# Kernel tuning notes

Hardware: AMD Instinct MI355X
Metric: run time of the kernel (lower is better)

## Reference

```python
import jax, jax.numpy as jnp
import numpy as np

G = 128          # voxel grid extent per axis
KS = 3           # kernel size per axis
KK = KS ** 3     # 27 kernel offsets
N_IN, N_OUT, C_IN, C_OUT = 50000, 100000, 128, 128


def setup_inputs() -> dict:
    key = jax.random.key(0)
    k1, k2, k3, k4 = jax.random.split(key, 4)
    features = jax.random.normal(k1, (N_IN, C_IN), dtype=jnp.float32)
    W = jax.random.normal(k2, (KK, C_IN, C_OUT), dtype=jnp.float32) * (1.0 / np.sqrt(C_IN * KK))
    inp_positions = jax.random.randint(k3, (N_IN, 3), 0, G, dtype=jnp.int32)
    out_positions = jax.random.randint(k4, (N_OUT, 3), 0, G, dtype=jnp.int32)
    return {"features": features, "W": W,
            "inp_positions": inp_positions, "out_positions": out_positions}


def _kernel_offsets():
    r = np.arange(KS) - KS // 2  # [-1, 0, 1] for KS=3 (offset=0 since KS is odd)
    dx, dy, dz = np.meshgrid(r, r, r, indexing="ij")
    return jnp.asarray(np.stack([dx.ravel(), dy.ravel(), dz.ravel()], axis=1), dtype=jnp.int32)  # [KK,3]


def reference(features, W, inp_positions, out_positions):
    # Sparse conv-transpose: voxelize input points (voxel_size=1, offset=0 -> identity
    # on integer coords), build voxel->input-index hash (dense grid table), then for
    # each output point gather the input feature at each of the KK kernel offsets and
    # accumulate W[k'] @ feat with mirrored kernel index (transpose of SparseConv).
    lin_in = (inp_positions[:, 0] * G + inp_positions[:, 1]) * G + inp_positions[:, 2]
    grid = jnp.full((G * G * G,), -1, dtype=jnp.int32)
    grid = grid.at[lin_in].max(jnp.arange(N_IN, dtype=jnp.int32))  # deterministic on dup voxels

    offsets = _kernel_offsets()          # [KK, 3]
    W_mirror = W[::-1]                   # transpose conv uses mirrored kernel index

    def step(acc, xk):
        off, Wk = xk                     # off [3], Wk [C_IN, C_OUT]
        nb = out_positions + off[None, :]               # [N_OUT, 3]
        in_bounds = jnp.all((nb >= 0) & (nb < G), axis=1)
        lin = (nb[:, 0] * G + nb[:, 1]) * G + nb[:, 2]
        idx = grid[jnp.clip(lin, 0, G * G * G - 1)]      # [N_OUT]
        ok = in_bounds & (idx >= 0)
        f = jnp.where(ok[:, None], features[jnp.clip(idx, 0)], 0.0)  # [N_OUT, C_IN]
        return acc + f @ Wk, None

    acc0 = jnp.zeros((out_positions.shape[0], W.shape[2]), dtype=features.dtype)
    out, _ = jax.lax.scan(step, acc0, (offsets, W_mirror))
    return out
```

## Files before the change

### kernel.cpp

```cpp
#include <hip/hip_runtime.h>
#include <hip/hip_bf16.h>

#define G    128
#define GGG  (G * G * G)
#define C    128
#define KK   27
#define CAP  4096
#define RT   16

typedef __attribute__((ext_vector_type(8))) short bf16x8;
typedef __attribute__((ext_vector_type(4))) float f32x4;

__device__ __forceinline__ ushort f2b(float f) {
    __hip_bfloat16 h = __float2bfloat16(f);
    return *reinterpret_cast<ushort*>(&h);
}

__global__ void prep_kernel(int4* __restrict__ grid4, int* __restrict__ cnt,
                            const float* __restrict__ W, ushort* __restrict__ Wtb) {
    int tid = blockIdx.x * blockDim.x + threadIdx.x;
    int stride = gridDim.x * blockDim.x;
    int4 mone = {-1, -1, -1, -1};
    for (int i = tid; i < GGG / 4; i += stride) grid4[i] = mone;
    if (tid < KK) cnt[tid] = 0;
    const int NW = KK * C * C;
    for (int i = tid; i < NW; i += stride) {
        int m = i >> 14;
        int r = i & 16383;
        int co = r >> 7, ci = r & 127;
        Wtb[i] = f2b(W[(size_t)(KK - 1 - m) * C * C + ci * C + co]);
    }
}

__global__ void scatter_kernel(const int* __restrict__ pos,
                               int* __restrict__ grid, int n) {
    int i = blockIdx.x * blockDim.x + threadIdx.x;
    if (i >= n) return;
    int x = pos[3 * i], y = pos[3 * i + 1], z = pos[3 * i + 2];
    atomicMax(&grid[(x * G + y) * G + z], i);
}

__global__ __launch_bounds__(256) void compact3b_kernel(
    const int* __restrict__ out_pos, const int* __restrict__ grid,
    int* __restrict__ cnt, int* __restrict__ pairs,
    int* __restrict__ cnt_row, int* __restrict__ rowtap, int n_out)
{
    int row = blockIdx.x * 256 + threadIdx.x;
    bool valid = row < n_out;
    int lane = threadIdx.x & 63;

    int px = 0, py = 0, pz = 0;
    if (valid) { px = out_pos[3*row]; py = out_pos[3*row+1]; pz = out_pos[3*row+2]; }

    int idx[KK];
#pragma unroll
    for (int m = 0; m < KK; ++m) {
        int x = px + m / 9 - 1, y = py + (m % 9) / 3 - 1, z = pz + m % 3 - 1;
        bool inb = valid && (unsigned)x < G && (unsigned)y < G && (unsigned)z < G;
        idx[m] = inb ? grid[(x * G + y) * G + z] : -1;
    }

    __shared__ int bcnt[KK], bbase[KK];
    if (threadIdx.x < KK) bcnt[threadIdx.x] = 0;
    __syncthreads();

    int gl[KK];
#pragma unroll
    for (int m = 0; m < KK; ++m) {
        unsigned long long act = __ballot(idx[m] >= 0);
        int lpre = __popcll(act & ((1ull << lane) - 1ull));
        int wcnt = __popcll(act);
        int wbase = 0;
        if (lane == 0 && wcnt) wbase = atomicAdd(&bcnt[m], wcnt);
        wbase = __shfl(wbase, 0);
        gl[m] = wbase + lpre;
    }
    __syncthreads();
    if (threadIdx.x < KK) bbase[threadIdx.x] = atomicAdd(&cnt[threadIdx.x], bcnt[threadIdx.x]);
    __syncthreads();

    int cr = 0;
#pragma unroll
    for (int m = 0; m < KK; ++m) {
        int g = -1;
        if (idx[m] >= 0) {
            g = bbase[m] + gl[m];
            if (g < CAP) pairs[m * CAP + g] = idx[m];
            else g = -1;
        }
        if (g >= 0 && cr < RT) {
            rowtap[cr * n_out + row] = (g << 5) | m;
            ++cr;
        }
    }
    if (valid) cnt_row[row] = cr;
}

__global__ __launch_bounds__(256, 3) void pair_mm3_kernel(
    const float* __restrict__ features, const ushort* __restrict__ Wtb,
    const int* __restrict__ pairs, const int* __restrict__ cnt,
    ushort* __restrict__ part)
{
    int m = blockIdx.y;
    int nm = min(cnt[m], CAP);
    if ((int)(blockIdx.x * 64) >= nm) return;

    __shared__ ushort Wl[128 * 136];
    __shared__ ushort Af[64 * 136];
    __shared__ int    idx_s[64];

    {
        const uint4* src = (const uint4*)(Wtb + (size_t)m * C * C);
        uint4* dst = (uint4*)Wl;
        for (int q = threadIdx.x; q < 2048; q += 256) {
            int r = q >> 4, c = q & 15;
            dst[r * 17 + c] = src[q];
        }
    }

    int lane = threadIdx.x & 63;
    int w    = threadIdx.x >> 6;
    int l15  = lane & 15;
    int quad = lane >> 4;
    const float4* fg4 = (const float4*)features;

    for (int base = blockIdx.x * 64; base < nm; base += gridDim.x * 64) {
        __syncthreads();
        if (threadIdx.x < 64) {
            int g = base + threadIdx.x;
            idx_s[threadIdx.x] = (g < nm) ? pairs[m * CAP + g] : -1;
        }
        __syncthreads();

#pragma unroll
        for (int k = 0; k < 8; ++k) {
            int q = threadIdx.x + k * 256;
            int r = q >> 5, c4 = q & 31;
            int id = idx_s[r];
            if (id >= 0) {
                float4 v = fg4[(size_t)id * 32 + c4];
                union { ushort u[4]; uint2 p; } pk;
                pk.u[0] = f2b(v.x); pk.u[1] = f2b(v.y);
                pk.u[2] = f2b(v.z); pk.u[3] = f2b(v.w);
                *(uint2*)&Af[r * 136 + c4 * 4] = pk.p;
            }
        }
        __syncthreads();

        f32x4 acc[8];
#pragma unroll
        for (int n = 0; n < 8; ++n) acc[n] = (f32x4){0.f, 0.f, 0.f, 0.f};

        int arow = 16 * w + l15;
#pragma unroll
        for (int kk = 0; kk < 4; ++kk) {
            bf16x8 a = *(bf16x8*)&Af[arow * 136 + kk * 32 + quad * 8];
#pragma unroll
            for (int n = 0; n < 8; ++n) {
                bf16x8 b = *(bf16x8*)&Wl[(n * 16 + l15) * 136 + kk * 32 + quad * 8];
                acc[n] = __builtin_amdgcn_mfma_f32_16x16x32_bf16(a, b, acc[n], 0, 0, 0);
            }
        }

        int r0 = 16 * w + quad * 4;
#pragma unroll
        for (int n = 0; n < 8; ++n) {
#pragma unroll
            for (int reg = 0; reg < 4; ++reg) {
                int r = r0 + reg;
                if (base + r < nm)
                    part[((size_t)(m * CAP + base + r)) * C + n * 16 + l15] =
                        f2b(acc[n][reg]);
            }
        }
    }
}

__global__ __launch_bounds__(256) void gather_sum2_kernel(
    const ushort* __restrict__ part, const int* __restrict__ rowtap,
    const int* __restrict__ cnt_row, float* __restrict__ out, int n_out)
{
    int row0 = blockIdx.x * 16;
    int rl = threadIdx.x >> 4;
    int t  = threadIdx.x & 15;
    int row = row0 + rl;

    __shared__ int rt_s[RT][16];
    __shared__ int cnt_s[16];
    if (threadIdx.x < 16) {
        int r = row0 + threadIdx.x;
        cnt_s[threadIdx.x] = (r < n_out) ? cnt_row[r] : 0;
    }
    {
        int q = threadIdx.x;
        int k = q >> 4, r = q & 15;
        rt_s[k][r] = (row0 + r < n_out) ? rowtap[k * n_out + row0 + r] : 0;
    }
    __syncthreads();

    int nt = cnt_s[rl];
    float acc[8] = {0,0,0,0,0,0,0,0};
    for (int k = 0; k < nt; ++k) {
        int e = rt_s[k][rl];
        int m = e & 31, g = e >> 5;
        uint4 v = *(const uint4*)(part + ((size_t)(m * CAP + g)) * C + t * 8);
        acc[0] += __uint_as_float(v.x << 16);
        acc[1] += __uint_as_float(v.x & 0xffff0000u);
        acc[2] += __uint_as_float(v.y << 16);
        acc[3] += __uint_as_float(v.y & 0xffff0000u);
        acc[4] += __uint_as_float(v.z << 16);
        acc[5] += __uint_as_float(v.z & 0xffff0000u);
        acc[6] += __uint_as_float(v.w << 16);
        acc[7] += __uint_as_float(v.w & 0xffff0000u);
    }
    if (row < n_out) {
        float* o = out + (size_t)row * C + t * 8;
        *(float4*)(o)     = (float4){acc[0], acc[1], acc[2], acc[3]};
        *(float4*)(o + 4) = (float4){acc[4], acc[5], acc[6], acc[7]};
    }
}

__global__ void init2_kernel(int4* __restrict__ grid4, int* __restrict__ cnt) {
    int i = blockIdx.x * blockDim.x + threadIdx.x;
    int stride = gridDim.x * blockDim.x;
    int4 mone = {-1, -1, -1, -1};
    for (int j = i; j < GGG / 4; j += stride) grid4[j] = mone;
    if (i < KK) cnt[i] = 0;
}

__global__ __launch_bounds__(128) void gather_mm_kernel(
    const float* __restrict__ features, const float* __restrict__ W,
    const int* __restrict__ out_pos, const int* __restrict__ grid,
    float* __restrict__ out, int n_out)
{
    int row = blockIdx.x;
    if (row >= n_out) return;
    int c = threadIdx.x;
    __shared__ int   nb_idx[KK];
    __shared__ float feat_s[C];
    int px = out_pos[3*row], py = out_pos[3*row+1], pz = out_pos[3*row+2];
    if (c < KK) {
        int i = c / 9, j = (c % 9) / 3, k = c % 3;
        int x = px + i - 1, y = py + j - 1, z = pz + k - 1;
        int idx = -1;
        if ((unsigned)x < G && (unsigned)y < G && (unsigned)z < G)
            idx = grid[(x * G + y) * G + z];
        nb_idx[c] = idx;
    }
    __syncthreads();
    float acc = 0.f;
    for (int m = 0; m < KK; ++m) {
        int idx = nb_idx[m];
        if (idx < 0) continue;
        __syncthreads();
        feat_s[c] = features[idx * C + c];
        __syncthreads();
        const float* __restrict__ Wk = W + (KK - 1 - m) * C * C + c;
        float a = 0.f;
#pragma unroll
        for (int ci = 0; ci < C; ++ci) a += feat_s[ci] * Wk[ci * C];
        acc += a;
    }
    out[row * C + c] = acc;
}

extern "C" void kernel_launch(void* const* d_in, const int* in_sizes, int n_in,
                              void* d_out, int out_size, void* d_ws, size_t ws_size,
                              hipStream_t stream) {
    const float* features = (const float*)d_in[0];
    const float* W        = (const float*)d_in[1];
    const int*   inp_pos  = (const int*)d_in[2];
    const int*   out_pos  = (const int*)d_in[3];
    float*       out      = (float*)d_out;

    int n_in_pts  = in_sizes[2] / 3;
    int n_out_pts = out_size / C;

    size_t o_grid   = 0;
    size_t o_cnt    = (size_t)GGG * 4;
    size_t o_pairs  = (o_cnt + 256 + 255) & ~(size_t)255;
    size_t o_cntr   = (o_pairs + (size_t)KK * CAP * 4 + 255) & ~(size_t)255;
    size_t o_rowtap = (o_cntr + (size_t)n_out_pts * 4 + 255) & ~(size_t)255;
    size_t o_wtb    = (o_rowtap + (size_t)RT * n_out_pts * 4 + 255) & ~(size_t)255;
    size_t o_part   = (o_wtb + (size_t)KK * C * C * 2 + 255) & ~(size_t)255;
    size_t need     = o_part + (size_t)KK * CAP * C * 2;

    int*    grid    = (int*)((char*)d_ws + o_grid);
    int*    cnt     = (int*)((char*)d_ws + o_cnt);
    int*    pairs   = (int*)((char*)d_ws + o_pairs);
    int*    cnt_row = (int*)((char*)d_ws + o_cntr);
    int*    rowtap  = (int*)((char*)d_ws + o_rowtap);
    ushort* Wtb     = (ushort*)((char*)d_ws + o_wtb);
    ushort* part    = (ushort*)((char*)d_ws + o_part);

    if (ws_size < need) {
        hipLaunchKernelGGL(init2_kernel, dim3(2048), dim3(256), 0, stream,
                           (int4*)grid, cnt);
        hipLaunchKernelGGL(scatter_kernel, dim3((n_in_pts + 255) / 256), dim3(256), 0, stream,
                           inp_pos, grid, n_in_pts);
        hipLaunchKernelGGL(gather_mm_kernel, dim3(n_out_pts), dim3(128), 0, stream,
                           features, W, out_pos, grid, out, n_out_pts);
        return;
    }

    hipLaunchKernelGGL(prep_kernel, dim3(1024), dim3(256), 0, stream,
                       (int4*)grid, cnt, W, Wtb);
    hipLaunchKernelGGL(scatter_kernel, dim3((n_in_pts + 255) / 256), dim3(256), 0, stream,
                       inp_pos, grid, n_in_pts);
    hipLaunchKernelGGL(compact3b_kernel, dim3((n_out_pts + 255) / 256), dim3(256), 0, stream,
                       out_pos, grid, cnt, pairs, cnt_row, rowtap, n_out_pts);
    hipLaunchKernelGGL(pair_mm3_kernel, dim3(40, KK), dim3(256), 0, stream,
                       features, Wtb, pairs, cnt, part);
    hipLaunchKernelGGL(gather_sum2_kernel, dim3((n_out_pts + 15) / 16), dim3(256), 0, stream,
                       part, rowtap, cnt_row, out, n_out_pts);
}
```

Before: 144.1 us.

## Shrink voxel grid to 16-bit and write single-tap rows directly to output

The voxel-to-input hash grid now stores 16-bit indices, written with a CAS-based 16-bit atomic max, which halves the grid memset and the lookup footprint. The pair list carries a destination row for output rows that have exactly one contributing tap. The MFMA kernel writes those rows straight to the fp32 output, skipping the bf16 partial buffer and the gather-sum pass for them. The gather kernel now loads only as many rowtap entries as the block's busiest row needs and skips single-tap rows. The 16-bit index assumes fewer than 65535 input points and uses CAS loops on shared words.

```diff
diff --git a/kernel.cpp b/kernel.cpp
--- a/kernel.cpp
+++ b/kernel.cpp
@@ -16,12 +16,12 @@
     return *reinterpret_cast<ushort*>(&h);
 }
 
-__global__ void prep_kernel(int4* __restrict__ grid4, int* __restrict__ cnt,
+__global__ void prep_kernel(uint4* __restrict__ grid16_4, int* __restrict__ cnt,
                             const float* __restrict__ W, ushort* __restrict__ Wtb) {
     int tid = blockIdx.x * blockDim.x + threadIdx.x;
     int stride = gridDim.x * blockDim.x;
-    int4 mone = {-1, -1, -1, -1};
-    for (int i = tid; i < GGG / 4; i += stride) grid4[i] = mone;
+    uint4 ffff = {0xFFFFFFFFu, 0xFFFFFFFFu, 0xFFFFFFFFu, 0xFFFFFFFFu};
+    for (int i = tid; i < GGG * 2 / 16; i += stride) grid16_4[i] = ffff;
     if (tid < KK) cnt[tid] = 0;
     const int NW = KK * C * C;
     for (int i = tid; i < NW; i += stride) {
@@ -32,17 +32,28 @@
     }
 }
 
-__global__ void scatter_kernel(const int* __restrict__ pos,
-                               int* __restrict__ grid, int n) {
+__global__ void scatter16_kernel(const int* __restrict__ pos,
+                                 unsigned int* __restrict__ gword, int n) {
     int i = blockIdx.x * blockDim.x + threadIdx.x;
     if (i >= n) return;
     int x = pos[3 * i], y = pos[3 * i + 1], z = pos[3 * i + 2];
-    atomicMax(&grid[(x * G + y) * G + z], i);
-}
-
-__global__ __launch_bounds__(256) void compact3b_kernel(
-    const int* __restrict__ out_pos, const int* __restrict__ grid,
-    int* __restrict__ cnt, int* __restrict__ pairs,
+    int lin = (x * G + y) * G + z;
+    unsigned int* w = &gword[lin >> 1];
+    int sh = (lin & 1) * 16;
+    unsigned int val = (unsigned int)i;
+    unsigned int old = *w, assumed;
+    do {
+        unsigned int cur = (old >> sh) & 0xFFFFu;
+        if (cur != 0xFFFFu && cur >= val) break;
+        unsigned int nw = (old & ~(0xFFFFu << sh)) | (val << sh);
+        assumed = old;
+        old = atomicCAS(w, assumed, nw);
+    } while (old != assumed);
+}
+
+__global__ __launch_bounds__(256) void compact4_kernel(
+    const int* __restrict__ out_pos, const ushort* __restrict__ grid16,
+    int* __restrict__ cnt, int2* __restrict__ pairs,
     int* __restrict__ cnt_row, int* __restrict__ rowtap, int n_out)
 {
     int row = blockIdx.x * 256 + threadIdx.x;
@@ -57,7 +68,8 @@
     for (int m = 0; m < KK; ++m) {
         int x = px + m / 9 - 1, y = py + (m % 9) / 3 - 1, z = pz + m % 3 - 1;
         bool inb = valid && (unsigned)x < G && (unsigned)y < G && (unsigned)z < G;
-        idx[m] = inb ? grid[(x * G + y) * G + z] : -1;
+        int v = inb ? (int)grid16[(x * G + y) * G + z] : 0xFFFF;
+        idx[m] = (v == 0xFFFF) ? -1 : v;
     }
 
     __shared__ int bcnt[KK], bbase[KK];
@@ -79,27 +91,36 @@
     if (threadIdx.x < KK) bbase[threadIdx.x] = atomicAdd(&cnt[threadIdx.x], bcnt[threadIdx.x]);
     __syncthreads();
 
+    int gs[KK];
     int cr = 0;
 #pragma unroll
     for (int m = 0; m < KK; ++m) {
         int g = -1;
         if (idx[m] >= 0) {
             g = bbase[m] + gl[m];
-            if (g < CAP) pairs[m * CAP + g] = idx[m];
-            else g = -1;
-        }
-        if (g >= 0 && cr < RT) {
-            rowtap[cr * n_out + row] = (g << 5) | m;
-            ++cr;
+            if (g >= CAP) g = -1;
+        }
+        gs[m] = g;
+        if (g >= 0) ++cr;
+    }
+
+    int dest = (cr == 1) ? row : -1;
+    int k = 0;
+#pragma unroll
+    for (int m = 0; m < KK; ++m) {
+        int g = gs[m];
+        if (g >= 0) {
+            pairs[m * CAP + g] = make_int2(idx[m], dest);
+            if (k < RT) { rowtap[k * n_out + row] = (g << 5) | m; ++k; }
         }
     }
     if (valid) cnt_row[row] = cr;
 }
 
-__global__ __launch_bounds__(256, 3) void pair_mm3_kernel(
+__global__ __launch_bounds__(256, 3) void pair_mm4_kernel(
     const float* __restrict__ features, const ushort* __restrict__ Wtb,
-    const int* __restrict__ pairs, const int* __restrict__ cnt,
-    ushort* __restrict__ part)
+    const int2* __restrict__ pairs, const int* __restrict__ cnt,
+    ushort* __restrict__ part, float* __restrict__ out)
 {
     int m = blockIdx.y;
     int nm = min(cnt[m], CAP);
@@ -108,6 +129,7 @@
     __shared__ ushort Wl[128 * 136];
     __shared__ ushort Af[64 * 136];
     __shared__ int    idx_s[64];
+    __shared__ int    dest_s[64];
 
     {
         const uint4* src = (const uint4*)(Wtb + (size_t)m * C * C);
@@ -128,7 +150,9 @@
         __syncthreads();
         if (threadIdx.x < 64) {
             int g = base + threadIdx.x;
-            idx_s[threadIdx.x] = (g < nm) ? pairs[m * CAP + g] : -1;
+            int2 pr = (g < nm) ? pairs[m * CAP + g] : make_int2(-1, -1);
+            idx_s[threadIdx.x]  = pr.x;
+            dest_s[threadIdx.x] = pr.y;
         }
         __syncthreads();
 
@@ -164,19 +188,24 @@
 
         int r0 = 16 * w + quad * 4;
 #pragma unroll
-        for (int n = 0; n < 8; ++n) {
-#pragma unroll
-            for (int reg = 0; reg < 4; ++reg) {
-                int r = r0 + reg;
-                if (base + r < nm)
-                    part[((size_t)(m * CAP + base + r)) * C + n * 16 + l15] =
-                        f2b(acc[n][reg]);
+        for (int reg = 0; reg < 4; ++reg) {
+            int r = r0 + reg;
+            if (base + r >= nm) continue;
+            int d = dest_s[r];
+            if (d >= 0) {
+                float* o = out + (size_t)d * C + l15;
+#pragma unroll
+                for (int n = 0; n < 8; ++n) o[n * 16] = acc[n][reg];
+            } else {
+                ushort* p = part + ((size_t)(m * CAP + base + r)) * C + l15;
+#pragma unroll
+                for (int n = 0; n < 8; ++n) p[n * 16] = f2b(acc[n][reg]);
             }
         }
     }
 }
 
-__global__ __launch_bounds__(256) void gather_sum2_kernel(
+__global__ __launch_bounds__(256) void gather_sum3_kernel(
     const ushort* __restrict__ part, const int* __restrict__ rowtap,
     const int* __restrict__ cnt_row, float* __restrict__ out, int n_out)
 {
@@ -187,18 +216,29 @@
 
     __shared__ int rt_s[RT][16];
     __shared__ int cnt_s[16];
+    __shared__ int maxc;
     if (threadIdx.x < 16) {
         int r = row0 + threadIdx.x;
         cnt_s[threadIdx.x] = (r < n_out) ? cnt_row[r] : 0;
     }
+    __syncthreads();
+    if (threadIdx.x == 0) {
+        int mx = 0;
+#pragma unroll
+        for (int i = 0; i < 16; ++i) mx = max(mx, cnt_s[i]);
+        maxc = mx;
+    }
+    __syncthreads();
     {
-        int q = threadIdx.x;
-        int k = q >> 4, r = q & 15;
-        rt_s[k][r] = (row0 + r < n_out) ? rowtap[k * n_out + row0 + r] : 0;
+        int k = threadIdx.x >> 4, r = threadIdx.x & 15;
+        if (k < maxc)
+            rt_s[k][r] = (row0 + r < n_out) ? rowtap[k * n_out + row0 + r] : 0;
     }
     __syncthreads();
 
     int nt = cnt_s[rl];
+    if (nt == 1) return;
+
     float acc[8] = {0,0,0,0,0,0,0,0};
     for (int k = 0; k < nt; ++k) {
         int e = rt_s[k][rl];
@@ -226,6 +266,14 @@
     int4 mone = {-1, -1, -1, -1};
     for (int j = i; j < GGG / 4; j += stride) grid4[j] = mone;
     if (i < KK) cnt[i] = 0;
+}
+
+__global__ void scatter_kernel(const int* __restrict__ pos,
+                               int* __restrict__ grid, int n) {
+    int i = blockIdx.x * blockDim.x + threadIdx.x;
+    if (i >= n) return;
+    int x = pos[3 * i], y = pos[3 * i + 1], z = pos[3 * i + 2];
+    atomicMax(&grid[(x * G + y) * G + z], i);
 }
 
 __global__ __launch_bounds__(128) void gather_mm_kernel(
@@ -279,38 +327,39 @@
     size_t o_grid   = 0;
     size_t o_cnt    = (size_t)GGG * 4;
     size_t o_pairs  = (o_cnt + 256 + 255) & ~(size_t)255;
-    size_t o_cntr   = (o_pairs + (size_t)KK * CAP * 4 + 255) & ~(size_t)255;
+    size_t o_cntr   = (o_pairs + (size_t)KK * CAP * 8 + 255) & ~(size_t)255;
     size_t o_rowtap = (o_cntr + (size_t)n_out_pts * 4 + 255) & ~(size_t)255;
     size_t o_wtb    = (o_rowtap + (size_t)RT * n_out_pts * 4 + 255) & ~(size_t)255;
     size_t o_part   = (o_wtb + (size_t)KK * C * C * 2 + 255) & ~(size_t)255;
     size_t need     = o_part + (size_t)KK * CAP * C * 2;
 
-    int*    grid    = (int*)((char*)d_ws + o_grid);
+    ushort* grid16  = (ushort*)((char*)d_ws + o_grid);
     int*    cnt     = (int*)((char*)d_ws + o_cnt);
-    int*    pairs   = (int*)((char*)d_ws + o_pairs);
+    int2*   pairs   = (int2*)((char*)d_ws + o_pairs);
     int*    cnt_row = (int*)((char*)d_ws + o_cntr);
     int*    rowtap  = (int*)((char*)d_ws + o_rowtap);
     ushort* Wtb     = (ushort*)((char*)d_ws + o_wtb);
     ushort* part    = (ushort*)((char*)d_ws + o_part);
 
     if (ws_size < need) {
+        int* grid32 = (int*)d_ws;
         hipLaunchKernelGGL(init2_kernel, dim3(2048), dim3(256), 0, stream,
-                           (int4*)grid, cnt);
+                           (int4*)grid32, cnt);
         hipLaunchKernelGGL(scatter_kernel, dim3((n_in_pts + 255) / 256), dim3(256), 0, stream,
-                           inp_pos, grid, n_in_pts);
+                           inp_pos, grid32, n_in_pts);
         hipLaunchKernelGGL(gather_mm_kernel, dim3(n_out_pts), dim3(128), 0, stream,
-                           features, W, out_pos, grid, out, n_out_pts);
+                           features, W, out_pos, grid32, out, n_out_pts);
         return;
     }
 
     hipLaunchKernelGGL(prep_kernel, dim3(1024), dim3(256), 0, stream,
-                       (int4*)grid, cnt, W, Wtb);
-    hipLaunchKernelGGL(scatter_kernel, dim3((n_in_pts + 255) / 256), dim3(256), 0, stream,
-                       inp_pos, grid, n_in_pts);
-    hipLaunchKernelGGL(compact3b_kernel, dim3((n_out_pts + 255) / 256), dim3(256), 0, stream,
-                       out_pos, grid, cnt, pairs, cnt_row, rowtap, n_out_pts);
-    hipLaunchKernelGGL(pair_mm3_kernel, dim3(40, KK), dim3(256), 0, stream,
-                       features, Wtb, pairs, cnt, part);
-    hipLaunchKernelGGL(gather_sum2_kernel, dim3((n_out_pts + 15) / 16), dim3(256), 0, stream,
+                       (uint4*)grid16, cnt, W, Wtb);
+    hipLaunchKernelGGL(scatter16_kernel, dim3((n_in_pts + 255) / 256), dim3(256), 0, stream,
+                       inp_pos, (unsigned int*)grid16, n_in_pts);
+    hipLaunchKernelGGL(compact4_kernel, dim3((n_out_pts + 255) / 256), dim3(256), 0, stream,
+                       out_pos, grid16, cnt, pairs, cnt_row, rowtap, n_out_pts);
+    hipLaunchKernelGGL(pair_mm4_kernel, dim3(40, KK), dim3(256), 0, stream,
+                       features, Wtb, pairs, cnt, part, out);
+    hipLaunchKernelGGL(gather_sum3_kernel, dim3((n_out_pts + 15) / 16), dim3(256), 0, stream,
                        part, rowtap, cnt_row, out, n_out_pts);
 }
```

New measurement: 141.3 us. About the same (-2.0%).
